# Optimization experiments

Measured on AMD Instinct MI355X. Metric: run time of the kernel, lower is better.

The kernel has to match this reference:

```python
import jax, jax.numpy as jnp
import numpy as np

N = 100000
E = 1600000
D = 64        # HID_NODE_ENC == HID_EDGE_ENC
H = 128       # HIDDEN_NODE_ONE
EPS = 1e-5
NEG_SLOPE = 0.01


def _xavier(key, shape):
    fan_in, fan_out = shape[0], shape[1]
    limit = float(np.sqrt(6.0 / (fan_in + fan_out)))
    return jax.random.uniform(key, shape, jnp.float32, -limit, limit)


def setup_inputs() -> dict:
    key = jax.random.key(0)
    ks = jax.random.split(key, 10)
    x = jax.random.normal(ks[0], (N, D), jnp.float32)
    edge_index = jax.random.randint(ks[1], (2, E), 0, N, jnp.int64)
    edge_attr = jax.random.normal(ks[2], (E, D), jnp.float32)
    u = jax.random.normal(ks[3], (1, 16), jnp.float32)
    batch = jnp.zeros((N,), jnp.int64)
    b_init = jnp.float32(0.01)
    params = {
        # node_mlp_1: Lin(128->128), LeakyReLU, BN(128), Lin(128->128)
        "W1": _xavier(ks[4], (2 * D, H)), "b1": jnp.full((H,), b_init),
        "g1": jnp.ones((H,), jnp.float32), "be1": jnp.zeros((H,), jnp.float32),
        "W2": _xavier(ks[5], (H, H)), "b2": jnp.full((H,), b_init),
        # node_mlp_2: Lin(192->128), LeakyReLU, BN(128), Lin(128->64)
        "W3": _xavier(ks[6], (H + D, H)), "b3": jnp.full((H,), b_init),
        "g2": jnp.ones((H,), jnp.float32), "be2": jnp.zeros((H,), jnp.float32),
        "W4": _xavier(ks[7], (H, D)), "b4": jnp.full((D,), b_init),
    }
    return {"x": x, "edge_index": edge_index, "edge_attr": edge_attr,
            "u": u, "batch": batch, **params}


def _bn(h, gamma, beta):
    # BatchNorm1d in training mode: biased batch statistics
    mean = jnp.mean(h, axis=0)
    var = jnp.mean(jnp.square(h - mean), axis=0)
    return (h - mean) * jax.lax.rsqrt(var + EPS) * gamma + beta


def reference(x, edge_index, edge_attr, u, batch,
              W1, b1, g1, be1, W2, b2,
              W3, b3, g2, be2, W4, b4):
    row, col = edge_index[0], edge_index[1]
    # gather + concat: [E, 2D]
    h = jnp.concatenate([x[row], edge_attr], axis=1)
    # node_mlp_1
    h = jax.nn.leaky_relu(h @ W1 + b1, NEG_SLOPE)
    h = _bn(h, g1, be1)
    h = h @ W2 + b2                       # [E, H]
    # scatter_add by destination node
    agg = jax.ops.segment_sum(h, col, num_segments=x.shape[0])  # [N, H]
    # concat with node feats, node_mlp_2
    h2 = jnp.concatenate([x, agg], axis=1)  # [N, H+D]
    h2 = jax.nn.leaky_relu(h2 @ W3 + b3, NEG_SLOPE)
    h2 = _bn(h2, g2, be2)
    return h2 @ W4 + b4                    # [N, D]
```

## Files before the change

kernel.cpp:

```cpp
#include <hip/hip_runtime.h>

#define NN 100000
#define NE 1600000
#define NTILE_E (NE / 128)
#define NTILE_N 782

typedef __attribute__((ext_vector_type(4))) float f32x4;
typedef __attribute__((ext_vector_type(8))) short s16x8;

__device__ __forceinline__ unsigned short f2bf(float f) {
  unsigned u = __builtin_bit_cast(unsigned, f);
  u = (u + 0x7FFFu + ((u >> 16) & 1u)) >> 16;
  return (unsigned short)u;
}
__device__ __forceinline__ void pack4(float4 v, unsigned short* dst) {
  ushort4 h;
  h.x = f2bf(v.x); h.y = f2bf(v.y); h.z = f2bf(v.z); h.w = f2bf(v.w);
  *(ushort4*)dst = h;
}

__global__ void k0_prep(const float* __restrict__ W1, const float* __restrict__ W3,
                        unsigned short* __restrict__ W1bT, unsigned short* __restrict__ W3bT) {
  int i = blockIdx.x * 256 + threadIdx.x;
  if (i < 16384) {
    int n = i >> 7, k = i & 127;
    W1bT[i] = f2bf(W1[k * 128 + n]);
  } else if (i < 16384 + 24576) {
    int j = i - 16384;
    int n = j / 192, k = j % 192;
    W3bT[j] = f2bf(W3[k * 128 + n]);
  }
}

__global__ void k_hist(const int* __restrict__ eidx, int* __restrict__ hist) {
  int e = blockIdx.x * 256 + threadIdx.x;
  if (e < NE) atomicAdd(&hist[eidx[NE + e]], 1);
}

__global__ void k_scan(int* __restrict__ hist, float* __restrict__ cntF) {
  __shared__ int ssum[1024];
  const int t = threadIdx.x;
  const int base = t * 98;
  const int cl = (base >= NN) ? 0 : ((NN - base < 98) ? (NN - base) : 98);
  int s = 0;
  for (int i = 0; i < cl; i++) s += hist[base + i];
  ssum[t] = s;
  __syncthreads();
  for (int d = 1; d < 1024; d <<= 1) {
    int v = (t >= d) ? ssum[t - d] : 0;
    __syncthreads();
    ssum[t] += v;
    __syncthreads();
  }
  int run = (t == 0) ? 0 : ssum[t - 1];
  for (int i = 0; i < cl; i++) {
    int hv = hist[base + i];
    hist[base + i] = run;
    cntF[base + i] = (float)hv;
    run += hv;
  }
}

__global__ void k_scatter(const int* __restrict__ eidx, int* __restrict__ off,
                          int* __restrict__ colS, int* __restrict__ eaIdx) {
  int e = blockIdx.x * 256 + threadIdx.x;
  if (e < NE) {
    int c = eidx[NE + e];
    int p = atomicAdd(&off[c], 1);
    colS[p] = c;
    eaIdx[p] = e;
  }
}

__global__ __launch_bounds__(256, 2) void k1_edge(
    const float* __restrict__ x, const int* __restrict__ eidx,
    const float* __restrict__ ea, const unsigned short* __restrict__ W1bT,
    const float* __restrict__ b1, const int* __restrict__ colS,
    const int* __restrict__ eaIdx,
    float* __restrict__ S, float* __restrict__ stat1) {
  __shared__ __align__(16) unsigned short At[128][136];
  __shared__ __align__(16) float Hs1[128][68];
  __shared__ int rIdxS[128];
  __shared__ int eIdxS[128];
  __shared__ int colT[132];
  __shared__ float sred[256];
  float (*Hs0)[68] = (float (*)[68])At;

  const int tid = threadIdx.x;
  const int wave = tid >> 6, lane = tid & 63;
  const int l15 = lane & 15, quad = lane >> 4;
  const int rowbase = (wave >> 1) * 64;
  const int colbase = (wave & 1) * 64;

  s16x8 bfrag[4][4];
#pragma unroll
  for (int ct = 0; ct < 4; ct++)
#pragma unroll
    for (int ks = 0; ks < 4; ks++)
      bfrag[ct][ks] = *(const s16x8*)(W1bT + (colbase + ct * 16 + l15) * 128 + ks * 32 + quad * 8);

  float b1j[4];
#pragma unroll
  for (int ct = 0; ct < 4; ct++) b1j[ct] = b1[colbase + ct * 16 + l15];

  float lsum[4] = {0, 0, 0, 0}, lsq[4] = {0, 0, 0, 0};

  for (int tile = blockIdx.x; tile < NTILE_E; tile += gridDim.x) {
    const int eb = tile * 128;
    __syncthreads();
    if (tid < 128) {
      int e0 = eaIdx[eb + tid];
      eIdxS[tid] = e0;
      rIdxS[tid] = eidx[e0];
      colT[tid + 1] = colS[eb + tid];
    } else if (tid == 128) {
      colT[0] = (eb > 0) ? colS[eb - 1] : -1;
    } else if (tid == 129) {
      colT[129] = (eb + 128 < NE) ? colS[eb + 128] : -1;
    }
    __syncthreads();
#pragma unroll
    for (int i = 0; i < 8; i++) {
      int idx = tid + i * 256; int e = idx >> 4, c = idx & 15;
      float4 v = ((const float4*)x)[(size_t)rIdxS[e] * 16 + c];
      pack4(v, &At[e][c * 4]);
    }
#pragma unroll
    for (int i = 0; i < 8; i++) {
      int idx = tid + i * 256; int e = idx >> 4, c = idx & 15;
      float4 v = ((const float4*)ea)[(size_t)eIdxS[e] * 16 + c];
      pack4(v, &At[e][64 + c * 4]);
    }
    __syncthreads();

    f32x4 acc[4][4];
#pragma unroll
    for (int rt = 0; rt < 4; rt++)
#pragma unroll
      for (int ct = 0; ct < 4; ct++) acc[rt][ct] = (f32x4){0.f, 0.f, 0.f, 0.f};

#pragma unroll
    for (int ks = 0; ks < 4; ks++) {
      s16x8 af[4];
#pragma unroll
      for (int rt = 0; rt < 4; rt++)
        af[rt] = *(const s16x8*)&At[rowbase + rt * 16 + l15][ks * 32 + quad * 8];
#pragma unroll
      for (int rt = 0; rt < 4; rt++)
#pragma unroll
        for (int ct = 0; ct < 4; ct++)
          acc[rt][ct] = __builtin_amdgcn_mfma_f32_16x16x32_bf16(af[rt], bfrag[ct][ks], acc[rt][ct], 0, 0, 0);
    }

    __syncthreads();
    {
      float (*H)[68] = (wave & 1) ? Hs1 : Hs0;
#pragma unroll
      for (int rt = 0; rt < 4; rt++)
#pragma unroll
        for (int r = 0; r < 4; r++) {
          const int er = rowbase + rt * 16 + quad * 4 + r;
#pragma unroll
          for (int ct = 0; ct < 4; ct++) {
            float v = acc[rt][ct][r] + b1j[ct];
            v = v > 0.0f ? v : 0.01f * v;
            lsum[ct] += v; lsq[ct] += v * v;
            H[er][ct * 16 + l15] = v;
          }
        }
    }
    __syncthreads();

    {
      const int col = tid & 63;
      const int r0 = (tid >> 6) * 32;
#pragma unroll
      for (int h = 0; h < 2; h++) {
        float (*H)[68] = h ? Hs1 : Hs0;
        float runsum = H[r0][col];
        int runstart = r0;
        int curnode = colT[r0 + 1];
        for (int r = r0 + 1; r < r0 + 32; ++r) {
          int nd = colT[r + 1];
          float v = H[r][col];
          if (nd == curnode) { runsum += v; }
          else {
            float* p = S + (size_t)curnode * 128 + h * 64 + col;
            if (colT[runstart] != curnode) *p = runsum;
            else atomicAdd(p, runsum);
            curnode = nd; runsum = v; runstart = r;
          }
        }
        float* p = S + (size_t)curnode * 128 + h * 64 + col;
        if (colT[runstart] != curnode && colT[r0 + 33] != curnode) *p = runsum;
        else atomicAdd(p, runsum);
      }
    }
  }

  sred[tid] = 0.0f;
  __syncthreads();
#pragma unroll
  for (int ct = 0; ct < 4; ct++) {
    float s = lsum[ct], q = lsq[ct];
    s += __shfl_down(s, 32); q += __shfl_down(q, 32);
    s += __shfl_down(s, 16); q += __shfl_down(q, 16);
    if (lane < 16) {
      atomicAdd(&sred[colbase + ct * 16 + l15], s);
      atomicAdd(&sred[128 + colbase + ct * 16 + l15], q);
    }
  }
  __syncthreads();
  atomicAdd(&stat1[tid], sred[tid]);
}

__global__ void k2_fold1(const float* __restrict__ stat1, const float* __restrict__ g1,
                         const float* __restrict__ be1, const float* __restrict__ W2,
                         const float* __restrict__ b2,
                         unsigned short* __restrict__ W2pT, float* __restrict__ v128) {
  __shared__ float s1s[128], t1s[128];
  __shared__ float red[256];
  const int tid = threadIdx.x;
  if (tid < 128) {
    float mean = stat1[tid] * (1.0f / NE);
    float var = stat1[128 + tid] * (1.0f / NE) - mean * mean;
    float rstd = rsqrtf(var + 1e-5f);
    float s = g1[tid] * rstd;
    s1s[tid] = s; t1s[tid] = be1[tid] - mean * s;
  }
  __syncthreads();
  const int b = blockIdx.x;
  if (b < 16) {
#pragma unroll
    for (int j = 0; j < 4; j++) {
      int i = b * 1024 + j * 256 + tid;
      int k = i >> 7, n = i & 127;
      W2pT[n * 128 + k] = f2bf(s1s[k] * W2[i]);
    }
  } else {
    int j = tid & 127, hh = tid >> 7;
    float p = 0.f;
    for (int k = hh * 64; k < hh * 64 + 64; k++) p += t1s[k] * W2[k * 128 + j];
    red[tid] = p;
    __syncthreads();
    if (tid < 128) v128[tid] = red[tid] + red[tid + 128] + b2[tid];
  }
}

__global__ __launch_bounds__(256, 2) void k3_node(
    const float* __restrict__ x, const float* __restrict__ S, const float* __restrict__ cnt,
    const unsigned short* __restrict__ W2pT, const float* __restrict__ v128,
    const unsigned short* __restrict__ W3bT, const float* __restrict__ b3,
    unsigned short* __restrict__ tOut, float* __restrict__ stat2) {
  __shared__ unsigned short Abuf[128][136];
  __shared__ unsigned short Xbuf[128][72];
  __shared__ float cbuf[128];
  __shared__ float sred[256];

  const int tid = threadIdx.x;
  const int wave = tid >> 6, lane = tid & 63;
  const int l15 = lane & 15, quad = lane >> 4;
  const int rowbase = (wave >> 1) * 64;
  const int colbase = (wave & 1) * 64;

  float vj[4], b3j[4];
#pragma unroll
  for (int ct = 0; ct < 4; ct++) {
    int jc = colbase + ct * 16 + l15;
    vj[ct] = v128[jc]; b3j[ct] = b3[jc];
  }
  float lsum[4] = {0, 0, 0, 0}, lsq[4] = {0, 0, 0, 0};

  for (int t = blockIdx.x; t < NTILE_N; t += gridDim.x) {
    const int nb = t * 128;
    __syncthreads();
#pragma unroll
    for (int i = 0; i < 16; i++) {
      int idx = tid + i * 256; int e = idx >> 5, c = idx & 31;
      int node = nb + e;
      float4 v = {0.f, 0.f, 0.f, 0.f};
      if (node < NN) v = ((const float4*)S)[(size_t)node * 32 + c];
      pack4(v, &Abuf[e][c * 4]);
    }
#pragma unroll
    for (int i = 0; i < 8; i++) {
      int idx = tid + i * 256; int e = idx >> 4, c = idx & 15;
      int node = nb + e;
      float4 v = {0.f, 0.f, 0.f, 0.f};
      if (node < NN) v = ((const float4*)x)[(size_t)node * 16 + c];
      pack4(v, &Xbuf[e][c * 4]);
    }
    if (tid < 128) cbuf[tid] = (nb + tid < NN) ? cnt[nb + tid] : 0.0f;
    __syncthreads();

    f32x4 acc[4][4];
#pragma unroll
    for (int rt = 0; rt < 4; rt++)
#pragma unroll
      for (int ct = 0; ct < 4; ct++) acc[rt][ct] = (f32x4){0.f, 0.f, 0.f, 0.f};
#pragma unroll
    for (int ks = 0; ks < 4; ks++) {
      s16x8 af[4];
#pragma unroll
      for (int rt = 0; rt < 4; rt++)
        af[rt] = *(const s16x8*)&Abuf[rowbase + rt * 16 + l15][ks * 32 + quad * 8];
      s16x8 bfr[4];
#pragma unroll
      for (int ct = 0; ct < 4; ct++)
        bfr[ct] = *(const s16x8*)(W2pT + (colbase + ct * 16 + l15) * 128 + ks * 32 + quad * 8);
#pragma unroll
      for (int rt = 0; rt < 4; rt++)
#pragma unroll
        for (int ct = 0; ct < 4; ct++)
          acc[rt][ct] = __builtin_amdgcn_mfma_f32_16x16x32_bf16(af[rt], bfr[ct], acc[rt][ct], 0, 0, 0);
    }
    __syncthreads();
#pragma unroll
    for (int rt = 0; rt < 4; rt++)
#pragma unroll
      for (int r = 0; r < 4; r++) {
        int er = rowbase + rt * 16 + quad * 4 + r;
#pragma unroll
        for (int ct = 0; ct < 4; ct++) {
          float val = acc[rt][ct][r] + cbuf[er] * vj[ct];
          Abuf[er][colbase + ct * 16 + l15] = f2bf(val);
        }
      }
    __syncthreads();

    f32x4 acc2[4][4];
#pragma unroll
    for (int rt = 0; rt < 4; rt++)
#pragma unroll
      for (int ct = 0; ct < 4; ct++) acc2[rt][ct] = (f32x4){0.f, 0.f, 0.f, 0.f};
#pragma unroll
    for (int ks = 0; ks < 6; ks++) {
      s16x8 af[4];
      if (ks < 2) {
#pragma unroll
        for (int rt = 0; rt < 4; rt++)
          af[rt] = *(const s16x8*)&Xbuf[rowbase + rt * 16 + l15][ks * 32 + quad * 8];
      } else {
#pragma unroll
        for (int rt = 0; rt < 4; rt++)
          af[rt] = *(const s16x8*)&Abuf[rowbase + rt * 16 + l15][(ks - 2) * 32 + quad * 8];
      }
      s16x8 bfr[4];
#pragma unroll
      for (int ct = 0; ct < 4; ct++)
        bfr[ct] = *(const s16x8*)(W3bT + (size_t)(colbase + ct * 16 + l15) * 192 + ks * 32 + quad * 8);
#pragma unroll
      for (int rt = 0; rt < 4; rt++)
#pragma unroll
        for (int ct = 0; ct < 4; ct++)
          acc2[rt][ct] = __builtin_amdgcn_mfma_f32_16x16x32_bf16(af[rt], bfr[ct], acc2[rt][ct], 0, 0, 0);
    }

#pragma unroll
    for (int rt = 0; rt < 4; rt++)
#pragma unroll
      for (int r = 0; r < 4; r++) {
        int er = rowbase + rt * 16 + quad * 4 + r;
        int node = nb + er;
        if (node < NN) {
#pragma unroll
          for (int ct = 0; ct < 4; ct++) {
            float val = acc2[rt][ct][r] + b3j[ct];
            val = val > 0.0f ? val : 0.01f * val;
            lsum[ct] += val; lsq[ct] += val * val;
            tOut[(size_t)node * 128 + colbase + ct * 16 + l15] = f2bf(val);
          }
        }
      }
  }

  sred[tid] = 0.0f;
  __syncthreads();
#pragma unroll
  for (int ct = 0; ct < 4; ct++) {
    float s = lsum[ct], q = lsq[ct];
    s += __shfl_down(s, 32); q += __shfl_down(q, 32);
    s += __shfl_down(s, 16); q += __shfl_down(q, 16);
    if (lane < 16) {
      atomicAdd(&sred[colbase + ct * 16 + l15], s);
      atomicAdd(&sred[128 + colbase + ct * 16 + l15], q);
    }
  }
  __syncthreads();
  atomicAdd(&stat2[tid], sred[tid]);
}

__global__ void k5_fold2(const float* __restrict__ stat2, const float* __restrict__ g2,
                         const float* __restrict__ be2, const float* __restrict__ W4,
                         const float* __restrict__ b4,
                         unsigned short* __restrict__ W4fT, float* __restrict__ b4f) {
  __shared__ float s2s[128], t2s[128];
  __shared__ float red[256];
  const int tid = threadIdx.x;
  if (tid < 128) {
    float mean = stat2[tid] * (1.0f / NN);
    float var = stat2[128 + tid] * (1.0f / NN) - mean * mean;
    float rstd = rsqrtf(var + 1e-5f);
    float s = g2[tid] * rstd;
    s2s[tid] = s; t2s[tid] = be2[tid] - mean * s;
  }
  __syncthreads();
  const int b = blockIdx.x;
  if (b < 8) {
#pragma unroll
    for (int j = 0; j < 4; j++) {
      int i = b * 1024 + j * 256 + tid;
      int k = i >> 6, n = i & 63;
      W4fT[n * 128 + k] = f2bf(s2s[k] * W4[i]);
    }
  } else {
    int j = tid & 63, part = tid >> 6;
    float p = 0.f;
    for (int k = part * 32; k < part * 32 + 32; k++) p += t2s[k] * W4[k * 64 + j];
    red[tid] = p;
    __syncthreads();
    if (tid < 64) b4f[tid] = red[tid] + red[tid + 64] + red[tid + 128] + red[tid + 192] + b4[tid];
  }
}

__global__ __launch_bounds__(256, 2) void k6_out(
    const unsigned short* __restrict__ tIn, const unsigned short* __restrict__ W4fT,
    const float* __restrict__ b4f, float* __restrict__ out) {
  __shared__ unsigned short Abuf[128][136];
  const int tid = threadIdx.x;
  const int wave = tid >> 6, lane = tid & 63;
  const int l15 = lane & 15, quad = lane >> 4;
  const int rowbase = (wave >> 1) * 64;
  const int colbase = (wave & 1) * 32;

  s16x8 bfrag[2][4];
#pragma unroll
  for (int ct = 0; ct < 2; ct++)
#pragma unroll
    for (int ks = 0; ks < 4; ks++)
      bfrag[ct][ks] = *(const s16x8*)(W4fT + (colbase + ct * 16 + l15) * 128 + ks * 32 + quad * 8);
  float bj[2];
#pragma unroll
  for (int ct = 0; ct < 2; ct++) bj[ct] = b4f[colbase + ct * 16 + l15];

  for (int t = blockIdx.x; t < NTILE_N; t += gridDim.x) {
    const int nb = t * 128;
    __syncthreads();
#pragma unroll
    for (int i = 0; i < 8; i++) {
      int idx = tid + i * 256; int e = idx >> 4, c = idx & 15;
      int node = nb + e;
      s16x8 v = {0, 0, 0, 0, 0, 0, 0, 0};
      if (node < NN) v = *(const s16x8*)(tIn + (size_t)node * 128 + c * 8);
      *(s16x8*)&Abuf[e][c * 8] = v;
    }
    __syncthreads();

    f32x4 acc[4][2];
#pragma unroll
    for (int rt = 0; rt < 4; rt++)
#pragma unroll
      for (int ct = 0; ct < 2; ct++) acc[rt][ct] = (f32x4){0.f, 0.f, 0.f, 0.f};
#pragma unroll
    for (int ks = 0; ks < 4; ks++) {
      s16x8 af[4];
#pragma unroll
      for (int rt = 0; rt < 4; rt++)
        af[rt] = *(const s16x8*)&Abuf[rowbase + rt * 16 + l15][ks * 32 + quad * 8];
#pragma unroll
      for (int rt = 0; rt < 4; rt++)
#pragma unroll
        for (int ct = 0; ct < 2; ct++)
          acc[rt][ct] = __builtin_amdgcn_mfma_f32_16x16x32_bf16(af[rt], bfrag[ct][ks], acc[rt][ct], 0, 0, 0);
    }
#pragma unroll
    for (int rt = 0; rt < 4; rt++)
#pragma unroll
      for (int r = 0; r < 4; r++) {
        int er = rowbase + rt * 16 + quad * 4 + r;
        int node = nb + er;
        if (node < NN) {
#pragma unroll
          for (int ct = 0; ct < 2; ct++)
            out[(size_t)node * 64 + colbase + ct * 16 + l15] = acc[rt][ct][r] + bj[ct];
        }
      }
  }
}

extern "C" void kernel_launch(void* const* d_in, const int* in_sizes, int n_in,
                              void* d_out, int out_size, void* d_ws, size_t ws_size,
                              hipStream_t stream) {
  (void)in_sizes; (void)n_in; (void)out_size; (void)ws_size;
  const float* x   = (const float*)d_in[0];
  const int*   ei  = (const int*)d_in[1];
  const float* ea  = (const float*)d_in[2];
  const float* W1  = (const float*)d_in[5];
  const float* b1  = (const float*)d_in[6];
  const float* g1  = (const float*)d_in[7];
  const float* be1 = (const float*)d_in[8];
  const float* W2  = (const float*)d_in[9];
  const float* b2  = (const float*)d_in[10];
  const float* W3  = (const float*)d_in[11];
  const float* b3  = (const float*)d_in[12];
  const float* g2  = (const float*)d_in[13];
  const float* be2 = (const float*)d_in[14];
  const float* W4  = (const float*)d_in[15];
  const float* b4  = (const float*)d_in[16];
  float* out = (float*)d_out;

  char* w = (char*)d_ws;
  float* S     = (float*)(w);
  float* stat1 = (float*)(w + 51200000);
  float* stat2 = (float*)(w + 51201024);
  int*   hist  = (int*)  (w + 51202048);
  float* cntF  = (float*)(w + 51602432);
  unsigned short* W1bT = (unsigned short*)(w + 52002816);
  unsigned short* W3bT = (unsigned short*)(w + 52035584);
  unsigned short* W2pT = (unsigned short*)(w + 52084736);
  float* v128  = (float*)(w + 52117504);
  unsigned short* W4fT = (unsigned short*)(w + 52118016);
  float* b4f   = (float*)(w + 52134400);
  unsigned short* tOut = (unsigned short*)(w + 52134656);
  int* colS  = (int*)(w + 52134656);
  int* eaIdx = (int*)(w + 58534656);

  hipMemsetAsync(d_ws, 0, 51602432, stream);

  k0_prep<<<160, 256, 0, stream>>>(W1, W3, W1bT, W3bT);
  k_hist<<<6250, 256, 0, stream>>>(ei, hist);
  k_scan<<<1, 1024, 0, stream>>>(hist, cntF);
  k_scatter<<<6250, 256, 0, stream>>>(ei, hist, colS, eaIdx);
  k1_edge<<<512, 256, 0, stream>>>(x, ei, ea, W1bT, b1, colS, eaIdx, S, stat1);
  k2_fold1<<<17, 256, 0, stream>>>(stat1, g1, be1, W2, b2, W2pT, v128);
  k3_node<<<512, 256, 0, stream>>>(x, S, cntF, W2pT, v128, W3bT, b3, tOut, stat2);
  k5_fold2<<<9, 256, 0, stream>>>(stat2, g2, be2, W4, b4, W4fT, b4f);
  k6_out<<<512, 256, 0, stream>>>(tOut, W4fT, b4f, out);
}
```

Before: 1.230 ms.

## Pack scatter pairs, widen edge kernel to 512 threads, unify node buffers

The separate colS/eaIdx arrays are merged into one int2 pair array, so the edge kernel reads one 8-byte record per edge instead of two scattered ints. The edge kernel now runs 512 threads per block, each wave handling 32 rows instead of 64, to raise occupancy and latency hiding on the gathers. Its H staging becomes a single 128-wide float tile, so each thread does one segmented-scan pass instead of two. The node kernel merges the x and aggregate buffers into one 200-wide LDS tile, and launch bounds for k3 and k6 are raised, which risks register spilling.

Measured after the change: 1.414 ms. +15.0%, slower.

```diff
diff --git a/kernel.cpp b/kernel.cpp
--- a/kernel.cpp
+++ b/kernel.cpp
@@ -62,34 +62,32 @@
 }
 
 __global__ void k_scatter(const int* __restrict__ eidx, int* __restrict__ off,
-                          int* __restrict__ colS, int* __restrict__ eaIdx) {
+                          int2* __restrict__ pairS) {
   int e = blockIdx.x * 256 + threadIdx.x;
   if (e < NE) {
     int c = eidx[NE + e];
     int p = atomicAdd(&off[c], 1);
-    colS[p] = c;
-    eaIdx[p] = e;
-  }
-}
-
-__global__ __launch_bounds__(256, 2) void k1_edge(
+    pairS[p] = make_int2(c, e);
+  }
+}
+
+__global__ __launch_bounds__(512, 4) void k1_edge(
     const float* __restrict__ x, const int* __restrict__ eidx,
     const float* __restrict__ ea, const unsigned short* __restrict__ W1bT,
-    const float* __restrict__ b1, const int* __restrict__ colS,
-    const int* __restrict__ eaIdx,
+    const float* __restrict__ b1, const int2* __restrict__ pairS,
     float* __restrict__ S, float* __restrict__ stat1) {
-  __shared__ __align__(16) unsigned short At[128][136];
-  __shared__ __align__(16) float Hs1[128][68];
+  __shared__ __align__(16) char HAt[67584];
   __shared__ int rIdxS[128];
   __shared__ int eIdxS[128];
   __shared__ int colT[132];
   __shared__ float sred[256];
-  float (*Hs0)[68] = (float (*)[68])At;
+  unsigned short (*At)[136] = (unsigned short (*)[136])HAt;
+  float (*H)[132] = (float (*)[132])HAt;
 
   const int tid = threadIdx.x;
   const int wave = tid >> 6, lane = tid & 63;
   const int l15 = lane & 15, quad = lane >> 4;
-  const int rowbase = (wave >> 1) * 64;
+  const int rowbase = (wave >> 1) * 32;
   const int colbase = (wave & 1) * 64;
 
   s16x8 bfrag[4][4];
@@ -109,96 +107,89 @@
     const int eb = tile * 128;
     __syncthreads();
     if (tid < 128) {
-      int e0 = eaIdx[eb + tid];
-      eIdxS[tid] = e0;
-      rIdxS[tid] = eidx[e0];
-      colT[tid + 1] = colS[eb + tid];
+      int2 pr = pairS[eb + tid];
+      eIdxS[tid] = pr.y;
+      rIdxS[tid] = eidx[pr.y];
+      colT[tid + 1] = pr.x;
     } else if (tid == 128) {
-      colT[0] = (eb > 0) ? colS[eb - 1] : -1;
+      colT[0] = (eb > 0) ? pairS[eb - 1].x : -1;
     } else if (tid == 129) {
-      colT[129] = (eb + 128 < NE) ? colS[eb + 128] : -1;
-    }
-    __syncthreads();
-#pragma unroll
-    for (int i = 0; i < 8; i++) {
-      int idx = tid + i * 256; int e = idx >> 4, c = idx & 15;
+      colT[129] = (eb + 128 < NE) ? pairS[eb + 128].x : -1;
+    }
+    __syncthreads();
+#pragma unroll
+    for (int i = 0; i < 4; i++) {
+      int idx = tid + i * 512; int e = idx >> 4, c = idx & 15;
       float4 v = ((const float4*)x)[(size_t)rIdxS[e] * 16 + c];
       pack4(v, &At[e][c * 4]);
     }
 #pragma unroll
-    for (int i = 0; i < 8; i++) {
-      int idx = tid + i * 256; int e = idx >> 4, c = idx & 15;
+    for (int i = 0; i < 4; i++) {
+      int idx = tid + i * 512; int e = idx >> 4, c = idx & 15;
       float4 v = ((const float4*)ea)[(size_t)eIdxS[e] * 16 + c];
       pack4(v, &At[e][64 + c * 4]);
     }
     __syncthreads();
 
-    f32x4 acc[4][4];
-#pragma unroll
-    for (int rt = 0; rt < 4; rt++)
+    f32x4 acc[2][4];
+#pragma unroll
+    for (int rt = 0; rt < 2; rt++)
 #pragma unroll
       for (int ct = 0; ct < 4; ct++) acc[rt][ct] = (f32x4){0.f, 0.f, 0.f, 0.f};
 
 #pragma unroll
     for (int ks = 0; ks < 4; ks++) {
-      s16x8 af[4];
-#pragma unroll
-      for (int rt = 0; rt < 4; rt++)
+      s16x8 af[2];
+#pragma unroll
+      for (int rt = 0; rt < 2; rt++)
         af[rt] = *(const s16x8*)&At[rowbase + rt * 16 + l15][ks * 32 + quad * 8];
 #pragma unroll
-      for (int rt = 0; rt < 4; rt++)
+      for (int rt = 0; rt < 2; rt++)
 #pragma unroll
         for (int ct = 0; ct < 4; ct++)
           acc[rt][ct] = __builtin_amdgcn_mfma_f32_16x16x32_bf16(af[rt], bfrag[ct][ks], acc[rt][ct], 0, 0, 0);
     }
 
     __syncthreads();
+#pragma unroll
+    for (int rt = 0; rt < 2; rt++)
+#pragma unroll
+      for (int r = 0; r < 4; r++) {
+        const int er = rowbase + rt * 16 + quad * 4 + r;
+#pragma unroll
+        for (int ct = 0; ct < 4; ct++) {
+          float v = acc[rt][ct][r] + b1j[ct];
+          v = v > 0.0f ? v : 0.01f * v;
+          lsum[ct] += v; lsq[ct] += v * v;
+          H[er][colbase + ct * 16 + l15] = v;
+        }
+      }
+    __syncthreads();
+
     {
-      float (*H)[68] = (wave & 1) ? Hs1 : Hs0;
-#pragma unroll
-      for (int rt = 0; rt < 4; rt++)
-#pragma unroll
-        for (int r = 0; r < 4; r++) {
-          const int er = rowbase + rt * 16 + quad * 4 + r;
-#pragma unroll
-          for (int ct = 0; ct < 4; ct++) {
-            float v = acc[rt][ct][r] + b1j[ct];
-            v = v > 0.0f ? v : 0.01f * v;
-            lsum[ct] += v; lsq[ct] += v * v;
-            H[er][ct * 16 + l15] = v;
-          }
+      const int col = tid & 127;
+      const int r0 = (tid >> 7) * 32;
+      float runsum = H[r0][col];
+      int runstart = r0;
+      int curnode = colT[r0 + 1];
+      for (int r = r0 + 1; r < r0 + 32; ++r) {
+        int nd = colT[r + 1];
+        float v = H[r][col];
+        if (nd == curnode) { runsum += v; }
+        else {
+          float* p = S + (size_t)curnode * 128 + col;
+          if (colT[runstart] != curnode) *p = runsum;
+          else atomicAdd(p, runsum);
+          curnode = nd; runsum = v; runstart = r;
         }
-    }
-    __syncthreads();
-
-    {
-      const int col = tid & 63;
-      const int r0 = (tid >> 6) * 32;
-#pragma unroll
-      for (int h = 0; h < 2; h++) {
-        float (*H)[68] = h ? Hs1 : Hs0;
-        float runsum = H[r0][col];
-        int runstart = r0;
-        int curnode = colT[r0 + 1];
-        for (int r = r0 + 1; r < r0 + 32; ++r) {
-          int nd = colT[r + 1];
-          float v = H[r][col];
-          if (nd == curnode) { runsum += v; }
-          else {
-            float* p = S + (size_t)curnode * 128 + h * 64 + col;
-            if (colT[runstart] != curnode) *p = runsum;
-            else atomicAdd(p, runsum);
-            curnode = nd; runsum = v; runstart = r;
-          }
-        }
-        float* p = S + (size_t)curnode * 128 + h * 64 + col;
-        if (colT[runstart] != curnode && colT[r0 + 33] != curnode) *p = runsum;
-        else atomicAdd(p, runsum);
       }
-    }
-  }
-
-  sred[tid] = 0.0f;
+      float* p = S + (size_t)curnode * 128 + col;
+      if (colT[runstart] != curnode && colT[r0 + 33] != curnode) *p = runsum;
+      else atomicAdd(p, runsum);
+    }
+  }
+
+  if (tid < 256) sred[tid] = 0.0f;
   __syncthreads();
 #pragma unroll
   for (int ct = 0; ct < 4; ct++) {
@@ -211,7 +202,7 @@
     }
   }
   __syncthreads();
-  atomicAdd(&stat1[tid], sred[tid]);
+  if (tid < 256) atomicAdd(&stat1[tid], sred[tid]);
 }
 
 __global__ void k2_fold1(const float* __restrict__ stat1, const float* __restrict__ g1,
@@ -247,13 +238,12 @@
   }
 }
 
-__global__ __launch_bounds__(256, 2) void k3_node(
+__global__ __launch_bounds__(256, 3) void k3_node(
     const float* __restrict__ x, const float* __restrict__ S, const float* __restrict__ cnt,
     const unsigned short* __restrict__ W2pT, const float* __restrict__ v128,
     const unsigned short* __restrict__ W3bT, const float* __restrict__ b3,
     unsigned short* __restrict__ tOut, float* __restrict__ stat2) {
-  __shared__ unsigned short Abuf[128][136];
-  __shared__ unsigned short Xbuf[128][72];
+  __shared__ __align__(16) unsigned short Abuf[128][200];
   __shared__ float cbuf[128];
   __shared__ float sred[256];
 
@@ -275,20 +265,20 @@
     const int nb = t * 128;
     __syncthreads();
 #pragma unroll
+    for (int i = 0; i < 8; i++) {
+      int idx = tid + i * 256; int e = idx >> 4, c = idx & 15;
+      int node = nb + e;
+      float4 v = {0.f, 0.f, 0.f, 0.f};
+      if (node < NN) v = ((const float4*)x)[(size_t)node * 16 + c];
+      pack4(v, &Abuf[e][c * 4]);
+    }
+#pragma unroll
     for (int i = 0; i < 16; i++) {
       int idx = tid + i * 256; int e = idx >> 5, c = idx & 31;
       int node = nb + e;
       float4 v = {0.f, 0.f, 0.f, 0.f};
       if (node < NN) v = ((const float4*)S)[(size_t)node * 32 + c];
-      pack4(v, &Abuf[e][c * 4]);
-    }
-#pragma unroll
-    for (int i = 0; i < 8; i++) {
-      int idx = tid + i * 256; int e = idx >> 4, c = idx & 15;
-      int node = nb + e;
-      float4 v = {0.f, 0.f, 0.f, 0.f};
-      if (node < NN) v = ((const float4*)x)[(size_t)node * 16 + c];
-      pack4(v, &Xbuf[e][c * 4]);
+      pack4(v, &Abuf[e][64 + c * 4]);
     }
     if (tid < 128) cbuf[tid] = (nb + tid < NN) ? cnt[nb + tid] : 0.0f;
     __syncthreads();
@@ -303,7 +293,7 @@
       s16x8 af[4];
 #pragma unroll
       for (int rt = 0; rt < 4; rt++)
-        af[rt] = *(const s16x8*)&Abuf[rowbase + rt * 16 + l15][ks * 32 + quad * 8];
+        af[rt] = *(const s16x8*)&Abuf[rowbase + rt * 16 + l15][64 + ks * 32 + quad * 8];
       s16x8 bfr[4];
 #pragma unroll
       for (int ct = 0; ct < 4; ct++)
@@ -323,7 +313,7 @@
 #pragma unroll
         for (int ct = 0; ct < 4; ct++) {
           float val = acc[rt][ct][r] + cbuf[er] * vj[ct];
-          Abuf[er][colbase + ct * 16 + l15] = f2bf(val);
+          Abuf[er][64 + colbase + ct * 16 + l15] = f2bf(val);
         }
       }
     __syncthreads();
@@ -336,15 +326,9 @@
 #pragma unroll
     for (int ks = 0; ks < 6; ks++) {
       s16x8 af[4];
-      if (ks < 2) {
-#pragma unroll
-        for (int rt = 0; rt < 4; rt++)
-          af[rt] = *(const s16x8*)&Xbuf[rowbase + rt * 16 + l15][ks * 32 + quad * 8];
-      } else {
-#pragma unroll
-        for (int rt = 0; rt < 4; rt++)
-          af[rt] = *(const s16x8*)&Abuf[rowbase + rt * 16 + l15][(ks - 2) * 32 + quad * 8];
-      }
+#pragma unroll
+      for (int rt = 0; rt < 4; rt++)
+        af[rt] = *(const s16x8*)&Abuf[rowbase + rt * 16 + l15][ks * 32 + quad * 8];
       s16x8 bfr[4];
 #pragma unroll
       for (int ct = 0; ct < 4; ct++)
@@ -423,7 +407,7 @@
   }
 }
 
-__global__ __launch_bounds__(256, 2) void k6_out(
+__global__ __launch_bounds__(256, 4) void k6_out(
     const unsigned short* __restrict__ tIn, const unsigned short* __restrict__ W4fT,
     const float* __restrict__ b4f, float* __restrict__ out) {
   __shared__ unsigned short Abuf[128][136];
@@ -522,16 +506,15 @@
   unsigned short* W4fT = (unsigned short*)(w + 52118016);
   float* b4f   = (float*)(w + 52134400);
   unsigned short* tOut = (unsigned short*)(w + 52134656);
-  int* colS  = (int*)(w + 52134656);
-  int* eaIdx = (int*)(w + 58534656);
+  int2* pairS = (int2*)(w + 52134656);
 
   hipMemsetAsync(d_ws, 0, 51602432, stream);
 
   k0_prep<<<160, 256, 0, stream>>>(W1, W3, W1bT, W3bT);
   k_hist<<<6250, 256, 0, stream>>>(ei, hist);
   k_scan<<<1, 1024, 0, stream>>>(hist, cntF);
-  k_scatter<<<6250, 256, 0, stream>>>(ei, hist, colS, eaIdx);
-  k1_edge<<<512, 256, 0, stream>>>(x, ei, ea, W1bT, b1, colS, eaIdx, S, stat1);
+  k_scatter<<<6250, 256, 0, stream>>>(ei, hist, pairS);
+  k1_edge<<<512, 512, 0, stream>>>(x, ei, ea, W1bT, b1, pairS, S, stat1);
   k2_fold1<<<17, 256, 0, stream>>>(stat1, g1, be1, W2, b2, W2pT, v128);
   k3_node<<<512, 256, 0, stream>>>(x, S, cntF, W2pT, v128, W3bT, b3, tOut, stat2);
   k5_fold2<<<9, 256, 0, stream>>>(stat2, g2, be2, W4, b4, W4fT, b4f);
```
